# Kernel tuning notes

Measured on AMD Instinct MI355X. Metric: run time of the kernel, lower is better.

The kernel has to match this reference:

```python
import jax, jax.numpy as jnp
import numpy as np

B, N, M = 4096, 128, 64
EPS_COS = 1e-8   # torch F.cosine_similarity default eps (clamp on norms)


def setup_inputs() -> dict:
    key = jax.random.key(0)
    ks = jax.random.split(key, 7)
    stdev = 1.0 / np.sqrt(N + M)
    # reset(): memory = abs(randn(N, M).repeat(B,1,1) * stdev); we draw per-batch which is equivalent math-wise
    memory = jnp.abs(jax.random.normal(ks[0], (B, N, M), jnp.float32) * stdev)
    k = jax.random.normal(ks[1], (B, M), jnp.float32)
    beta = jax.random.normal(ks[2], (B, 1), jnp.float32)
    g = jax.random.normal(ks[3], (B, 1), jnp.float32)
    s = jax.random.normal(ks[4], (B, 3), jnp.float32)
    gamma = jax.random.normal(ks[5], (B, 1), jnp.float32)
    # w_prev is a weighting from the previous step: a valid distribution over N rows
    w_prev = jax.nn.softmax(jax.random.normal(ks[6], (B, N), jnp.float32), axis=1)
    return {"memory": memory, "k": k, "beta": beta, "g": g, "s": s,
            "gamma": gamma, "w_prev": w_prev}


def reference(memory, k, beta, g, s, gamma, w_prev):
    # parameter squashing (ROM.address)
    beta = jax.nn.softplus(beta)              # [B,1] key strength > 0
    g = jax.nn.sigmoid(g)                     # [B,1] interpolation gate
    s = jax.nn.softmax(s, axis=1)             # [B,3] shift weighting
    gamma = 1.0 + jax.nn.softplus(gamma)      # [B,1] sharpen >= 1

    # _similarity: cosine similarity between memory rows and key, then softmax
    mem = memory + 1e-16                      # [B,N,M]
    kk = k + 1e-16                            # [B,M]
    dot = jnp.einsum('bnm,bm->bn', mem, kk)   # [B,N]
    mem_norm = jnp.maximum(jnp.linalg.norm(mem, axis=-1), EPS_COS)            # [B,N]
    key_norm = jnp.maximum(jnp.linalg.norm(kk, axis=-1, keepdims=True), EPS_COS)  # [B,1]
    wc = jax.nn.softmax(beta * (dot / (mem_norm * key_norm)), axis=1)         # [B,N]

    # _interpolate
    wg = g * wc + (1.0 - g) * w_prev          # [B,N]

    # _shift: batched circular 3-tap convolution (replaces per-batch conv1d loop)
    # c[i] = w[(i-1)%N]*s[0] + w[i]*s[1] + w[(i+1)%N]*s[2]
    w_hat = (jnp.roll(wg, 1, axis=1) * s[:, 0:1]
             + wg * s[:, 1:2]
             + jnp.roll(wg, -1, axis=1) * s[:, 2:3])

    # _sharpen
    w = w_hat ** gamma
    return w / (jnp.sum(w, axis=1, keepdims=True) + 1e-16)
```

## Files before the change

kernel.cpp:

```cpp
#include <hip/hip_runtime.h>
#include <hip/hip_bf16.h>


constexpr int ROM_N = 128;
constexpr int ROM_M = 64;
constexpr int N_IN  = 7;

__device__ __forceinline__ float bf2f(unsigned short u) {
    union { unsigned int i; float f; } v;
    v.i = ((unsigned int)u) << 16;
    return v.f;
}

__device__ __forceinline__ unsigned short f2bf(float f) {
    union { float f; unsigned int i; } v; v.f = f;
    unsigned int x = v.i;
    x += 0x7fffu + ((x >> 16) & 1u);
    return (unsigned short)(x >> 16);
}

__device__ __forceinline__ float waveReduceSum(float v) {
#pragma unroll
    for (int off = 32; off > 0; off >>= 1) v += __shfl_down(v, off, 64);
    return v;
}

__device__ __forceinline__ float waveReduceMax(float v) {
#pragma unroll
    for (int off = 32; off > 0; off >>= 1) v = fmaxf(v, __shfl_down(v, off, 64));
    return v;
}

struct DetectArgs {
    const void* p[N_IN];
    int n[N_IN];
};

__global__ void detect_kernel(DetectArgs a, int* flags) {
    const int t = threadIdx.x;
    int isf32 = 0;
    if (t < N_IN) {
        const unsigned short* u = (const unsigned short*)a.p[t];
        int c = a.n[t] < 64 ? a.n[t] : 64;
        for (int i = 0; i < c; ++i) {
            float v = bf2f(u[i]);
            if (!(fabsf(v) < 1e4f)) isf32 = 1;
        }
    }
    unsigned long long mask = __ballot(isf32 != 0);
    if (t == 0) {
        int f32mask = (int)(mask & 0x7Full);
        flags[0] = f32mask;
        flags[1] = (f32mask != 0x7F) ? 1 : 0;
    }
}

__device__ __forceinline__ float ld1(const void* p, size_t i, bool f32) {
    return f32 ? ((const float*)p)[i] : bf2f(((const unsigned short*)p)[i]);
}

__global__ __launch_bounds__(128) void rom_kernel(
    const void* __restrict__ memory,
    const void* __restrict__ kvec,
    const void* __restrict__ beta_in,
    const void* __restrict__ g_in,
    const void* __restrict__ s_in,
    const void* __restrict__ gamma_in,
    const void* __restrict__ wprev,
    void* __restrict__ outp,
    const int* __restrict__ flags)
{
    const int b = blockIdx.x;
    const int t = threadIdx.x;
    const int wave = t >> 6;
    const int lane = t & 63;

    const int fm = flags[0];
    const bool memF32 = (fm >> 0) & 1, kF32 = (fm >> 1) & 1, beF32 = (fm >> 2) & 1;
    const bool gF32 = (fm >> 3) & 1, sF32 = (fm >> 4) & 1, gaF32 = (fm >> 5) & 1;
    const bool wpF32 = (fm >> 6) & 1;
    const bool outBf = flags[1] != 0;

    __shared__ float kk[ROM_M];
    __shared__ float scal[6];
    __shared__ float keynorm;
    __shared__ float wredm[2], wreds[2], wredn[2];
    __shared__ float wgs[ROM_N];

    if (t < ROM_M) {
        float kv = ld1(kvec, (size_t)b * ROM_M + t, kF32) + 1e-16f;
        kk[t] = kv;
        float ss = waveReduceSum(kv * kv);
        if (t == 0) keynorm = fmaxf(sqrtf(ss), 1e-8f);
    }
    if (t == 64) {
        scal[0] = log1pf(expf(ld1(beta_in, b, beF32)));
        scal[1] = 1.0f / (1.0f + expf(-ld1(g_in, b, gF32)));
        float s0 = ld1(s_in, (size_t)b * 3 + 0, sF32);
        float s1 = ld1(s_in, (size_t)b * 3 + 1, sF32);
        float s2 = ld1(s_in, (size_t)b * 3 + 2, sF32);
        float mx = fmaxf(s0, fmaxf(s1, s2));
        float e0 = expf(s0 - mx), e1 = expf(s1 - mx), e2 = expf(s2 - mx);
        float inv = 1.0f / (e0 + e1 + e2);
        scal[2] = e0 * inv; scal[3] = e1 * inv; scal[4] = e2 * inv;
        scal[5] = 1.0f + log1pf(expf(ld1(gamma_in, b, gaF32)));
    }
    __syncthreads();

    float dot = 0.0f, ssq = 0.0f;
    const size_t rowOff = ((size_t)b * ROM_N + t) * ROM_M;
    if (memF32) {
        const float4* rv = reinterpret_cast<const float4*>((const float*)memory + rowOff);
#pragma unroll
        for (int i = 0; i < 16; ++i) {
            float4 q = rv[i];
            float a0 = q.x + 1e-16f, a1 = q.y + 1e-16f;
            float a2 = q.z + 1e-16f, a3 = q.w + 1e-16f;
            dot += a0 * kk[i*4] + a1 * kk[i*4+1] + a2 * kk[i*4+2] + a3 * kk[i*4+3];
            ssq += a0 * a0 + a1 * a1 + a2 * a2 + a3 * a3;
        }
    } else {
        const uint4* rv = reinterpret_cast<const uint4*>((const unsigned short*)memory + rowOff);
#pragma unroll
        for (int i = 0; i < 8; ++i) {
            uint4 p = rv[i];
            unsigned int wds[4] = {p.x, p.y, p.z, p.w};
#pragma unroll
            for (int j = 0; j < 4; ++j) {
                float lo = bf2f((unsigned short)(wds[j] & 0xffffu)) + 1e-16f;
                float hi = bf2f((unsigned short)(wds[j] >> 16)) + 1e-16f;
                int m0 = i * 8 + j * 2;
                dot += lo * kk[m0] + hi * kk[m0 + 1];
                ssq += lo * lo + hi * hi;
            }
        }
    }
    float mem_norm = fmaxf(sqrtf(ssq), 1e-8f);
    float x = scal[0] * (dot / (mem_norm * keynorm));

    float m = waveReduceMax(x);
    if (lane == 0) wredm[wave] = m;
    __syncthreads();
    float gmax = fmaxf(wredm[0], wredm[1]);
    float e = expf(x - gmax);
    float ps = waveReduceSum(e);
    if (lane == 0) wreds[wave] = ps;
    __syncthreads();
    float wc = e / (wreds[0] + wreds[1]);

    float g = scal[1];
    float wp = ld1(wprev, (size_t)b * ROM_N + t, wpF32);
    float wg = g * wc + (1.0f - g) * wp;
    wgs[t] = wg;
    __syncthreads();

    float wh = wgs[(t + ROM_N - 1) & (ROM_N - 1)] * scal[2]
             + wg * scal[3]
             + wgs[(t + 1) & (ROM_N - 1)] * scal[4];

    float w = powf(wh, scal[5]);
    float pn = waveReduceSum(w);
    if (lane == 0) wredn[wave] = pn;
    __syncthreads();
    float total = wredn[0] + wredn[1] + 1e-16f;
    float val = w / total;

    const size_t oi = (size_t)b * ROM_N + t;
    if (outBf) ((unsigned short*)outp)[oi] = f2bf(val);
    else       ((float*)outp)[oi] = val;
}

extern "C" void kernel_launch(void* const* d_in, const int* in_sizes, int n_in,
                              void* d_out, int out_size, void* d_ws, size_t ws_size,
                              hipStream_t stream) {
    DetectArgs da;
    for (int i = 0; i < N_IN; ++i) { da.p[i] = d_in[i]; da.n[i] = in_sizes[i]; }
    int* flags = (int*)d_ws;

    detect_kernel<<<1, 64, 0, stream>>>(da, flags);

    const int B = in_sizes[0] / (ROM_N * ROM_M);
    rom_kernel<<<B, ROM_N, 0, stream>>>(d_in[0], d_in[1], d_in[2], d_in[3],
                                        d_in[4], d_in[5], d_in[6], d_out, flags);
}
```

Measured before the change: 215.9 us.

## Coalesce memory reads via LDS partial sums and fold dtype detection into main kernel

Each thread previously read its own 256-byte memory row, giving strided, uncoalesced global loads. Now consecutive threads read consecutive 16-byte chunks, compute partial dot and sum-of-squares per chunk, and write them to a padded LDS buffer that each thread then reduces for its row. The separate dtype-detection launch is removed, and every block repeats the detection scan itself. This adds about 18KB of LDS per block and an extra barrier, and the per-block detection scan adds redundant small reads.

```diff
diff --git a/kernel.cpp b/kernel.cpp
--- a/kernel.cpp
+++ b/kernel.cpp
@@ -5,6 +5,7 @@
 constexpr int ROM_N = 128;
 constexpr int ROM_M = 64;
 constexpr int N_IN  = 7;
+constexpr int PSTR  = 36;
 
 __device__ __forceinline__ float bf2f(unsigned short u) {
     union { unsigned int i; float f; } v;
@@ -31,109 +32,104 @@
     return v;
 }
 
-struct DetectArgs {
-    const void* p[N_IN];
-    int n[N_IN];
-};
-
-__global__ void detect_kernel(DetectArgs a, int* flags) {
-    const int t = threadIdx.x;
-    int isf32 = 0;
-    if (t < N_IN) {
-        const unsigned short* u = (const unsigned short*)a.p[t];
-        int c = a.n[t] < 64 ? a.n[t] : 64;
-        for (int i = 0; i < c; ++i) {
-            float v = bf2f(u[i]);
-            if (!(fabsf(v) < 1e4f)) isf32 = 1;
-        }
-    }
-    unsigned long long mask = __ballot(isf32 != 0);
-    if (t == 0) {
-        int f32mask = (int)(mask & 0x7Full);
-        flags[0] = f32mask;
-        flags[1] = (f32mask != 0x7F) ? 1 : 0;
-    }
-}
+struct KArgs { const void* p[N_IN]; };
 
 __device__ __forceinline__ float ld1(const void* p, size_t i, bool f32) {
     return f32 ? ((const float*)p)[i] : bf2f(((const unsigned short*)p)[i]);
 }
 
-__global__ __launch_bounds__(128) void rom_kernel(
-    const void* __restrict__ memory,
-    const void* __restrict__ kvec,
-    const void* __restrict__ beta_in,
-    const void* __restrict__ g_in,
-    const void* __restrict__ s_in,
-    const void* __restrict__ gamma_in,
-    const void* __restrict__ wprev,
-    void* __restrict__ outp,
-    const int* __restrict__ flags)
-{
+__global__ __launch_bounds__(128) void rom_kernel(KArgs a, void* __restrict__ outp) {
     const int b = blockIdx.x;
     const int t = threadIdx.x;
     const int wave = t >> 6;
     const int lane = t & 63;
+    const int g16 = t & 15;
+    const int a16 = t >> 4;
 
-    const int fm = flags[0];
-    const bool memF32 = (fm >> 0) & 1, kF32 = (fm >> 1) & 1, beF32 = (fm >> 2) & 1;
-    const bool gF32 = (fm >> 3) & 1, sF32 = (fm >> 4) & 1, gaF32 = (fm >> 5) & 1;
-    const bool wpF32 = (fm >> 6) & 1;
-    const bool outBf = flags[1] != 0;
-
+    __shared__ int   sf[N_IN];
     __shared__ float kk[ROM_M];
     __shared__ float scal[6];
     __shared__ float keynorm;
     __shared__ float wredm[2], wreds[2], wredn[2];
     __shared__ float wgs[ROM_N];
+    __shared__ float part[ROM_N * PSTR];
+
+    if (t < N_IN) {
+        const unsigned short* u = (const unsigned short*)a.p[t];
+        int bad = 0;
+#pragma unroll
+        for (int i = 0; i < 64; ++i) {
+            float v = bf2f(u[i]);
+            if (!(fabsf(v) < 1e4f)) bad = 1;
+        }
+        sf[t] = bad;
+    }
+    __syncthreads();
+    int fm = 0;
+#pragma unroll
+    for (int j = 0; j < N_IN; ++j) fm |= sf[j] << j;
+    const bool memF32 = (fm >> 0) & 1, kF32 = (fm >> 1) & 1, beF32 = (fm >> 2) & 1;
+    const bool gF32 = (fm >> 3) & 1, sF32 = (fm >> 4) & 1, gaF32 = (fm >> 5) & 1;
+    const bool wpF32 = (fm >> 6) & 1;
+    const bool outBf = (fm != 0x7F);
 
     if (t < ROM_M) {
-        float kv = ld1(kvec, (size_t)b * ROM_M + t, kF32) + 1e-16f;
+        float kv = ld1(a.p[1], (size_t)b * ROM_M + t, kF32) + 1e-16f;
         kk[t] = kv;
         float ss = waveReduceSum(kv * kv);
         if (t == 0) keynorm = fmaxf(sqrtf(ss), 1e-8f);
     }
     if (t == 64) {
-        scal[0] = log1pf(expf(ld1(beta_in, b, beF32)));
-        scal[1] = 1.0f / (1.0f + expf(-ld1(g_in, b, gF32)));
-        float s0 = ld1(s_in, (size_t)b * 3 + 0, sF32);
-        float s1 = ld1(s_in, (size_t)b * 3 + 1, sF32);
-        float s2 = ld1(s_in, (size_t)b * 3 + 2, sF32);
+        scal[0] = log1pf(expf(ld1(a.p[2], b, beF32)));
+        scal[1] = 1.0f / (1.0f + expf(-ld1(a.p[3], b, gF32)));
+        float s0 = ld1(a.p[4], (size_t)b * 3 + 0, sF32);
+        float s1 = ld1(a.p[4], (size_t)b * 3 + 1, sF32);
+        float s2 = ld1(a.p[4], (size_t)b * 3 + 2, sF32);
         float mx = fmaxf(s0, fmaxf(s1, s2));
         float e0 = expf(s0 - mx), e1 = expf(s1 - mx), e2 = expf(s2 - mx);
         float inv = 1.0f / (e0 + e1 + e2);
         scal[2] = e0 * inv; scal[3] = e1 * inv; scal[4] = e2 * inv;
-        scal[5] = 1.0f + log1pf(expf(ld1(gamma_in, b, gaF32)));
+        scal[5] = 1.0f + log1pf(expf(ld1(a.p[5], b, gaF32)));
+    }
+    __syncthreads();
+
+    const float4 kcv = ((const float4*)kk)[g16];
+    if (memF32) {
+        const float4* mv = (const float4*)((const float*)a.p[0] + (size_t)b * (ROM_N * ROM_M));
+#pragma unroll
+        for (int i = 0; i < 16; ++i) {
+            float4 v = mv[t + 128 * i];
+            float a0 = v.x + 1e-16f, a1 = v.y + 1e-16f;
+            float a2 = v.z + 1e-16f, a3 = v.w + 1e-16f;
+            float d = a0 * kcv.x + a1 * kcv.y + a2 * kcv.z + a3 * kcv.w;
+            float s = a0 * a0 + a1 * a1 + a2 * a2 + a3 * a3;
+            int r = a16 + 8 * i;
+            ((float2*)part)[r * (PSTR / 2) + g16] = make_float2(d, s);
+        }
+    } else {
+        const uint2* mv = (const uint2*)((const unsigned short*)a.p[0] + (size_t)b * (ROM_N * ROM_M));
+#pragma unroll
+        for (int i = 0; i < 16; ++i) {
+            uint2 u = mv[t + 128 * i];
+            float a0 = bf2f((unsigned short)(u.x & 0xffffu)) + 1e-16f;
+            float a1 = bf2f((unsigned short)(u.x >> 16)) + 1e-16f;
+            float a2 = bf2f((unsigned short)(u.y & 0xffffu)) + 1e-16f;
+            float a3 = bf2f((unsigned short)(u.y >> 16)) + 1e-16f;
+            float d = a0 * kcv.x + a1 * kcv.y + a2 * kcv.z + a3 * kcv.w;
+            float s = a0 * a0 + a1 * a1 + a2 * a2 + a3 * a3;
+            int r = a16 + 8 * i;
+            ((float2*)part)[r * (PSTR / 2) + g16] = make_float2(d, s);
+        }
     }
     __syncthreads();
 
     float dot = 0.0f, ssq = 0.0f;
-    const size_t rowOff = ((size_t)b * ROM_N + t) * ROM_M;
-    if (memF32) {
-        const float4* rv = reinterpret_cast<const float4*>((const float*)memory + rowOff);
+    const float4* pr = (const float4*)(part + t * PSTR);
 #pragma unroll
-        for (int i = 0; i < 16; ++i) {
-            float4 q = rv[i];
-            float a0 = q.x + 1e-16f, a1 = q.y + 1e-16f;
-            float a2 = q.z + 1e-16f, a3 = q.w + 1e-16f;
-            dot += a0 * kk[i*4] + a1 * kk[i*4+1] + a2 * kk[i*4+2] + a3 * kk[i*4+3];
-            ssq += a0 * a0 + a1 * a1 + a2 * a2 + a3 * a3;
-        }
-    } else {
-        const uint4* rv = reinterpret_cast<const uint4*>((const unsigned short*)memory + rowOff);
-#pragma unroll
-        for (int i = 0; i < 8; ++i) {
-            uint4 p = rv[i];
-            unsigned int wds[4] = {p.x, p.y, p.z, p.w};
-#pragma unroll
-            for (int j = 0; j < 4; ++j) {
-                float lo = bf2f((unsigned short)(wds[j] & 0xffffu)) + 1e-16f;
-                float hi = bf2f((unsigned short)(wds[j] >> 16)) + 1e-16f;
-                int m0 = i * 8 + j * 2;
-                dot += lo * kk[m0] + hi * kk[m0 + 1];
-                ssq += lo * lo + hi * hi;
-            }
-        }
+    for (int j = 0; j < 8; ++j) {
+        float4 v = pr[j];
+        dot += v.x + v.z;
+        ssq += v.y + v.w;
     }
     float mem_norm = fmaxf(sqrtf(ssq), 1e-8f);
     float x = scal[0] * (dot / (mem_norm * keynorm));
@@ -149,7 +145,7 @@
     float wc = e / (wreds[0] + wreds[1]);
 
     float g = scal[1];
-    float wp = ld1(wprev, (size_t)b * ROM_N + t, wpF32);
+    float wp = ld1(a.p[6], (size_t)b * ROM_N + t, wpF32);
     float wg = g * wc + (1.0f - g) * wp;
     wgs[t] = wg;
     __syncthreads();
@@ -173,13 +169,8 @@
 extern "C" void kernel_launch(void* const* d_in, const int* in_sizes, int n_in,
                               void* d_out, int out_size, void* d_ws, size_t ws_size,
                               hipStream_t stream) {
-    DetectArgs da;
-    for (int i = 0; i < N_IN; ++i) { da.p[i] = d_in[i]; da.n[i] = in_sizes[i]; }
-    int* flags = (int*)d_ws;
-
-    detect_kernel<<<1, 64, 0, stream>>>(da, flags);
-
+    KArgs a;
+    for (int i = 0; i < N_IN; ++i) a.p[i] = d_in[i];
     const int B = in_sizes[0] / (ROM_N * ROM_M);
-    rom_kernel<<<B, ROM_N, 0, stream>>>(d_in[0], d_in[1], d_in[2], d_in[3],
-                                        d_in[4], d_in[5], d_in[6], d_out, flags);
+    rom_kernel<<<B, ROM_N, 0, stream>>>(a, d_out);
 }
```

Result: faster. 207.8 us (-3.8%).
